# Performance work log

Measured on AMD Instinct MI355X. Metric: run time of the kernel, lower is better.

## Reference

```python
import jax, jax.numpy as jnp
import numpy as np

H = 8          # attention heads
EPS = 1e-5     # LayerNorm eps (torch default)
B, T, E = 8, 1024, 128
D, DI, N, DC, R = 512, 1024, 16, 4, 32   # d_model, d_inner, d_state, d_conv, dt_rank
NT, NM = 6, 8                            # transformer layers, mamba layers
FF = 2048                                # transformer dim_feedforward (torch default)


def setup_inputs():
    key = jax.random.key(0)
    ks = iter(jax.random.split(key, 48))
    def rn(shape, scale=0.05):
        return jax.random.normal(next(ks), shape, jnp.float32) * scale
    return {
        "emb":      jax.random.normal(next(ks), (B, T, E), jnp.float32),
        # TransformerEncoder (6 post-norm layers), params stacked on leading layer dim
        "t_wqkv":   rn((NT, 3 * E, E)), "t_bqkv": jnp.zeros((NT, 3 * E), jnp.float32),
        "t_wo":     rn((NT, E, E)),     "t_bo":   jnp.zeros((NT, E), jnp.float32),
        "t_ln1w":   jnp.ones((NT, E), jnp.float32),  "t_ln1b": jnp.zeros((NT, E), jnp.float32),
        "t_w1":     rn((NT, FF, E)),    "t_b1":   jnp.zeros((NT, FF), jnp.float32),
        "t_w2":     rn((NT, E, FF)),    "t_b2":   jnp.zeros((NT, E), jnp.float32),
        "t_ln2w":   jnp.ones((NT, E), jnp.float32),  "t_ln2b": jnp.zeros((NT, E), jnp.float32),
        # Linear(emb_dim -> d_model)
        "w_in":     rn((D, E)), "b_in": jnp.zeros((D,), jnp.float32),
        # MambaBlocks (8 raw Mamba layers, no residual/norm), stacked
        "m_inproj": rn((NM, 2 * DI, D)),
        "m_convw":  rn((NM, DI, DC), 0.2), "m_convb": jnp.zeros((NM, DI), jnp.float32),
        "m_xproj":  rn((NM, R + 2 * N, DI)),
        "m_dtw":    rn((NM, DI, R), 0.1),
        "m_dtb":    jax.random.uniform(next(ks), (NM, DI), jnp.float32, -6.0, -3.0),
        "m_Alog":   jnp.log(jnp.tile(jnp.arange(1, N + 1, dtype=jnp.float32), (NM, DI, 1))),
        "m_D":      jnp.ones((NM, DI), jnp.float32),
        "m_outproj": rn((NM, D, DI)),
        # Linear(d_model -> emb_dim)
        "w_out":    rn((E, D)), "b_out": jnp.zeros((E,), jnp.float32),
    }


def _ln(x, w, b):
    mu = jnp.mean(x, -1, keepdims=True)
    var = jnp.var(x, -1, keepdims=True)
    return (x - mu) * jax.lax.rsqrt(var + EPS) * w + b


def _tlayer(x, p):
    wqkv, bqkv, wo, bo, ln1w, ln1b, w1, b1, w2, b2, ln2w, ln2b = p
    qkv = x @ wqkv.T + bqkv                        # (B,T,3E)
    q, k, v = jnp.split(qkv, 3, axis=-1)
    def heads(t):                                  # (B,T,E) -> (B,H,T,E//H)
        return t.reshape(B, T, H, E // H).transpose(0, 2, 1, 3)
    q, k, v = heads(q), heads(k), heads(v)
    scores = jnp.einsum("bhqd,bhkd->bhqk", q, k) / jnp.sqrt(jnp.float32(E // H))
    attn = jax.nn.softmax(scores, axis=-1)
    o = jnp.einsum("bhqk,bhkd->bhqd", attn, v).transpose(0, 2, 1, 3).reshape(B, T, E)
    x = _ln(x + o @ wo.T + bo, ln1w, ln1b)         # post-norm (torch default)
    ff = jax.nn.relu(x @ w1.T + b1) @ w2.T + b2
    return _ln(x + ff, ln2w, ln2b)


def _mamba_layer(x, p):
    inproj, convw, convb, xproj, dtw, dtb, Alog, Dp, outproj = p
    xz = x @ inproj.T                              # (B,T,2*DI)
    xi, z = jnp.split(xz, 2, axis=-1)
    # causal depthwise conv1d, kernel DC, left-padded
    xp = jnp.pad(xi, ((0, 0), (DC - 1, 0), (0, 0)))
    conv = sum(xp[:, k:k + T, :] * convw[:, k] for k in range(DC)) + convb
    xi = jax.nn.silu(conv)
    dbc = xi @ xproj.T                             # (B,T,R+2N)
    dt_r, Bt, Ct = dbc[..., :R], dbc[..., R:R + N], dbc[..., R + N:]
    dt = jax.nn.softplus(dt_r @ dtw.T + dtb)       # (B,T,DI)
    A = -jnp.exp(Alog)                             # (DI,N)
    def step(h, inputs):
        dt_t, B_t, C_t, x_t = inputs               # (B,DI),(B,N),(B,N),(B,DI)
        dA = jnp.exp(dt_t[:, :, None] * A)         # (B,DI,N)
        h = h * dA + (dt_t * x_t)[:, :, None] * B_t[:, None, :]
        y = jnp.einsum("bdn,bn->bd", h, C_t)
        return h, y
    h0 = jnp.zeros((B, DI, N), x.dtype)
    seq = (dt.transpose(1, 0, 2), Bt.transpose(1, 0, 2),
           Ct.transpose(1, 0, 2), xi.transpose(1, 0, 2))
    _, ys = jax.lax.scan(step, h0, seq)            # ys: (T,B,DI)
    y = ys.transpose(1, 0, 2) + Dp * xi
    y = y * jax.nn.silu(z)
    return y @ outproj.T                           # (B,T,D)


def reference(emb, t_wqkv, t_bqkv, t_wo, t_bo, t_ln1w, t_ln1b, t_w1, t_b1, t_w2, t_b2,
              t_ln2w, t_ln2b, w_in, b_in, m_inproj, m_convw, m_convb, m_xproj, m_dtw,
              m_dtb, m_Alog, m_D, m_outproj, w_out, b_out):
    x = emb
    tparams = (t_wqkv, t_bqkv, t_wo, t_bo, t_ln1w, t_ln1b, t_w1, t_b1, t_w2, t_b2, t_ln2w, t_ln2b)
    for i in range(NT):
        x = _tlayer(x, tuple(p[i] for p in tparams))
    x = x @ w_in.T + b_in                          # (B,T,D)
    mparams = (m_inproj, m_convw, m_convb, m_xproj, m_dtw, m_dtb, m_Alog, m_D, m_outproj)
    for i in range(NM):
        x = _mamba_layer(x, tuple(p[i] for p in mparams))
    return x @ w_out.T + b_out                     # (B,T,E)
```

## Files before the change

kernel.cpp:

```cpp
#include <hip/hip_runtime.h>
#include <math.h>

#define HB 8
#define TT 1024
#define NSTATE 16
#define NTT 6
#define NMM 8
#define MM (HB*TT)
#define EPSV 1e-5f
#define CHUNK 64
#define NCH (TT/CHUNK)
#define AKS 128
#define VSTR 132

typedef _Float16 f16x8 __attribute__((ext_vector_type(8)));
typedef _Float16 f16x4 __attribute__((ext_vector_type(4)));
typedef float f32x4_t __attribute__((ext_vector_type(4)));

static __device__ __forceinline__ void split8(const float4 a, const float4 b,
                                              f16x8& h, f16x8& l)
{
  float x[8] = {a.x, a.y, a.z, a.w, b.x, b.y, b.z, b.w};
#pragma unroll
  for (int i = 0; i < 8; i++) {
    _Float16 hi = (_Float16)x[i];
    h[i] = hi;
    l[i] = (_Float16)(x[i] - (float)hi);
  }
}

static __device__ __forceinline__ void gload16(const _Float16* g, _Float16* l)
{
  __builtin_amdgcn_global_load_lds(
      (const __attribute__((address_space(1))) unsigned int*)g,
      (__attribute__((address_space(3))) unsigned int*)l, 16, 0, 0);
}

static __device__ __forceinline__ void store_split(_Float16* __restrict__ dst,
                                                   size_t row, int col, float v)
{
  const int cc = col & 31;
  const size_t o = ((size_t)(col >> 5) * MM + row) * 64
                 + (size_t)(((((cc >> 3) ^ ((int)row & 7)) * 8)) + (cc & 7));
  _Float16 hi = (_Float16)v;
  dst[o] = hi;
  dst[o ^ (size_t)32] = (_Float16)(v - (float)hi);
}

static __device__ __forceinline__ void split_item(
    const float* __restrict__ src, int lda, int rows,
    _Float16* __restrict__ dst, int item)
{
  const int m = item % rows;
  const int seg = item / rows;
  const float* s = src + (size_t)m * lda + seg * 32;
  _Float16* d = dst + (size_t)item * 64;
  const int swz = m & 7;
#pragma unroll
  for (int g = 0; g < 4; g++) {
    float4 x0 = *(const float4*)&s[g * 8];
    float4 x1 = *(const float4*)&s[g * 8 + 4];
    f16x8 h, l;
    split8(x0, x1, h, l);
    const int u = (g ^ swz) * 8;
    *(f16x8*)&d[u] = h;
    *(f16x8*)&d[u ^ 32] = l;
  }
}

__global__ __launch_bounds__(256) void split_k(
    const float* __restrict__ src, int lda, int rows,
    _Float16* __restrict__ dst)
{
  split_item(src, lda, rows, dst, blockIdx.x * 256 + threadIdx.x);
}

__global__ __launch_bounds__(256) void split3_k(
    const float* __restrict__ s0, int lda0, int rows0, _Float16* __restrict__ d0, int nb0,
    const float* __restrict__ s1, int lda1, int rows1, _Float16* __restrict__ d1, int nb1,
    const float* __restrict__ s2, int lda2, int rows2, _Float16* __restrict__ d2)
{
  const int bid = blockIdx.x;
  if (bid < nb0) {
    split_item(s0, lda0, rows0, d0, bid * 256 + threadIdx.x);
  } else if (bid < nb0 + nb1) {
    split_item(s1, lda1, rows1, d1, (bid - nb0) * 256 + threadIdx.x);
  } else {
    split_item(s2, lda2, rows2, d2, (bid - nb0 - nb1) * 256 + threadIdx.x);
  }
}

template<int TN>
__global__ __launch_bounds__(256, 4) void gemm_ps_t(
    const _Float16* __restrict__ Ap, int astr,
    const _Float16* __restrict__ Wp, int wstr,
    const float* __restrict__ bias,
    float* __restrict__ C,
    float* __restrict__ P,
    _Float16* __restrict__ Cs,
    int N, int K, int S, int act)
{
  __shared__ __align__(16) _Float16 As[128 * 64];
  __shared__ __align__(16) _Float16 Bs[TN * 64];
  const int tid = threadIdx.x;
  const int lane = tid & 63;
  const int w = tid >> 6;
  const int quad = lane >> 4;
  const int l16 = lane & 15;
  const int m0 = blockIdx.y * 128;
  const int n0 = blockIdx.x * TN;
  const int z = blockIdx.z;
  const int nseg = K / 32;
  const int segb = z * (nseg / S);
  const int sege = segb + nseg / S;

  constexpr int MI = (TN == 128) ? 4 : 2;
  const int w0 = (TN == 128) ? (w & 1) : w;
  const int w1 = (TN == 128) ? (w >> 1) : 0;
  const int rowbase = (TN == 128) ? w0 * 64 : w0 * 32;

  f32x4_t acc[MI][4];
#pragma unroll
  for (int i = 0; i < MI; i++)
#pragma unroll
    for (int j = 0; j < 4; j++)
#pragma unroll
      for (int r = 0; r < 4; r++) acc[i][j][r] = 0.f;

  const int sw8 = (quad ^ (l16 & 7)) * 8;
  const int abase = (rowbase + l16) * 64 + sw8;
  const int bbase = (w1 * 64 + l16) * 64 + sw8;
  const int wave64 = tid & 192;

  for (int seg = segb; seg < sege; seg++) {
    const _Float16* At = Ap + ((size_t)seg * astr + m0) * 64;
    const _Float16* Bt = Wp + ((size_t)seg * wstr + n0) * 64;
    __syncthreads();
#pragma unroll
    for (int j = 0; j < 4; j++)
      gload16(At + (size_t)(j * 256 + tid) * 8, &As[(j * 256 + wave64) * 8]);
#pragma unroll
    for (int j = 0; j < TN / 32; j++)
      gload16(Bt + (size_t)(j * 256 + tid) * 8, &Bs[(j * 256 + wave64) * 8]);
    __syncthreads();

    f16x8 bh[4], bl[4];
#pragma unroll
    for (int ni = 0; ni < 4; ni++) {
      bh[ni] = *(const f16x8*)&Bs[bbase + ni * 1024];
      bl[ni] = *(const f16x8*)&Bs[(bbase ^ 32) + ni * 1024];
    }
#pragma unroll
    for (int mi = 0; mi < MI; mi++) {
      f16x8 ah = *(const f16x8*)&As[abase + mi * 1024];
      f16x8 al = *(const f16x8*)&As[(abase ^ 32) + mi * 1024];
#pragma unroll
      for (int ni = 0; ni < 4; ni++) {
        acc[mi][ni] = __builtin_amdgcn_mfma_f32_16x16x32_f16(ah, bh[ni], acc[mi][ni], 0, 0, 0);
        acc[mi][ni] = __builtin_amdgcn_mfma_f32_16x16x32_f16(ah, bl[ni], acc[mi][ni], 0, 0, 0);
        acc[mi][ni] = __builtin_amdgcn_mfma_f32_16x16x32_f16(al, bh[ni], acc[mi][ni], 0, 0, 0);
      }
    }
  }

  float* dst = (S == 1) ? C : (P + (size_t)z * MM * N);
#pragma unroll
  for (int ni = 0; ni < 4; ni++) {
    const int n = n0 + w1 * 64 + ni * 16 + l16;
    const float bv = (S == 1 && bias) ? bias[n] : 0.f;
#pragma unroll
    for (int mi = 0; mi < MI; mi++) {
      const int mbase = m0 + rowbase + mi * 16 + quad * 4;
#pragma unroll
      for (int r = 0; r < 4; r++) {
        float v = acc[mi][ni][r] + bv;
        if (S == 1) {
          if (act == 1) v = fmaxf(v, 0.f);
          else if (act == 2) v = fmaxf(v, 0.f) + log1pf(__expf(-fabsf(v)));
        }
        const int row = mbase + r;
        if (S == 1 && Cs) {
          store_split(Cs, (size_t)row, n, v);
        } else {
          dst[(size_t)row * N + n] = v;
        }
      }
    }
  }
}

__global__ __launch_bounds__(256) void reduce_k(
    const float* __restrict__ P, const float* __restrict__ bias,
    float* __restrict__ C, _Float16* __restrict__ Cs,
    _Float16* __restrict__ dta,
    int nmask, int nshift, int S, int act, int stride4)
{
  const int idx = blockIdx.x * 256 + threadIdx.x;
  float4 a = *(const float4*)&P[(size_t)idx * 4];
  for (int z = 1; z < S; z++) {
    float4 p = *(const float4*)&P[(size_t)(idx + (size_t)z * stride4) * 4];
    a.x += p.x; a.y += p.y; a.z += p.z; a.w += p.w;
  }
  if (bias) {
    float4 bv = *(const float4*)&bias[(idx * 4) & nmask];
    a.x += bv.x; a.y += bv.y; a.z += bv.z; a.w += bv.w;
  }
  if (act == 1) {
    a.x = fmaxf(a.x, 0.f); a.y = fmaxf(a.y, 0.f);
    a.z = fmaxf(a.z, 0.f); a.w = fmaxf(a.w, 0.f);
  } else if (act == 2) {
    a.x = fmaxf(a.x, 0.f) + log1pf(__expf(-fabsf(a.x)));
    a.y = fmaxf(a.y, 0.f) + log1pf(__expf(-fabsf(a.y)));
    a.z = fmaxf(a.z, 0.f) + log1pf(__expf(-fabsf(a.z)));
    a.w = fmaxf(a.w, 0.f) + log1pf(__expf(-fabsf(a.w)));
  }
  const int c0 = (idx * 4) & nmask;
  const size_t row = (size_t)(idx * 4) >> nshift;
  if (Cs) {
    store_split(Cs, row, c0,     a.x);
    store_split(Cs, row, c0 + 1, a.y);
    store_split(Cs, row, c0 + 2, a.z);
    store_split(Cs, row, c0 + 3, a.w);
  } else {
    *(float4*)&C[(size_t)idx * 4] = a;
  }
  if (dta && c0 < 32) {
    store_split(dta, row, c0,     a.x);
    store_split(dta, row, c0 + 1, a.y);
    store_split(dta, row, c0 + 2, a.z);
    store_split(dta, row, c0 + 3, a.w);
  }
}

__global__ __launch_bounds__(256) void attn_mfma_k(
    const float* __restrict__ qkv, _Float16* __restrict__ os)
{
  __shared__ _Float16 Khi[AKS * 16], Klo[AKS * 16];
  __shared__ _Float16 Vthi[16 * VSTR], Vtlo[16 * VSTR];
  __shared__ float Pscr[4][16 * 18];

  const int tid = threadIdx.x;
  const int lane = tid & 63;
  const int wv = tid >> 6;
  const int quad = lane >> 4;
  const int l16 = lane & 15;
  const int qh = quad & 1;
  const int bh = blockIdx.y;
  const int b = bh >> 3;
  const int h = bh & 7;
  const int qb0 = blockIdx.x * 128;

  f16x8 qa[2];
#pragma unroll
  for (int u = 0; u < 2; u++) {
    const int qrow = qb0 + wv * 32 + u * 16 + l16;
    const float* qp = qkv + (size_t)(b * TT + qrow) * 384 + h * 16 + qh * 8;
    float4 x0 = *(const float4*)&qp[0];
    float4 x1 = *(const float4*)&qp[4];
    float xv[8] = {x0.x, x0.y, x0.z, x0.w, x1.x, x1.y, x1.z, x1.w};
#pragma unroll
    for (int j = 0; j < 8; j++) {
      float q = xv[j] * 0.25f;
      _Float16 hi = (_Float16)q;
      _Float16 lo = (_Float16)(q - (float)hi);
      qa[u][j] = (quad < 2) ? hi : lo;
    }
  }

  f32x4_t oacc[2];
  float lacc[2][4];
#pragma unroll
  for (int u = 0; u < 2; u++)
#pragma unroll
    for (int r = 0; r < 4; r++) { oacc[u][r] = 0.f; lacc[u][r] = 0.f; }

  float* Pw = &Pscr[wv][0];

  for (int ks = 0; ks < TT; ks += AKS) {
    __syncthreads();
    {
      const int key = tid >> 1, hf = tid & 1;
      const float* kp = qkv + (size_t)(b * TT + ks + key) * 384 + 128 + h * 16 + hf * 8;
      float4 k0 = *(const float4*)&kp[0];
      float4 k1 = *(const float4*)&kp[4];
      f16x8 vh, vl;
      split8(k0, k1, vh, vl);
      *(f16x8*)&Khi[key * 16 + hf * 8] = vh;
      *(f16x8*)&Klo[key * 16 + hf * 8] = vl;
      const float* vp = kp + 128;
      float4 v0 = *(const float4*)&vp[0];
      float4 v1 = *(const float4*)&vp[4];
      float vvv[8] = {v0.x, v0.y, v0.z, v0.w, v1.x, v1.y, v1.z, v1.w};
#pragma unroll
      for (int j = 0; j < 8; j++) {
        const int d = hf * 8 + j;
        _Float16 hi = (_Float16)vvv[j];
        Vthi[d * VSTR + key] = hi;
        Vtlo[d * VSTR + key] = (_Float16)(vvv[j] - (float)hi);
      }
    }
    __syncthreads();

    for (int kt = 0; kt < AKS; kt += 16) {
      f16x8 kfh = *(const f16x8*)&Khi[(kt + l16) * 16 + qh * 8];
      f16x8 kfl = *(const f16x8*)&Klo[(kt + l16) * 16 + qh * 8];
      const int vo = l16 * VSTR + kt + qh * 8;
      f16x4 va0 = *(const f16x4*)&Vthi[vo];
      f16x4 va1 = *(const f16x4*)&Vthi[vo + 4];
      f16x4 vb0 = *(const f16x4*)&Vtlo[vo];
      f16x4 vb1 = *(const f16x4*)&Vtlo[vo + 4];
      f16x8 vfh, vfl;
#pragma unroll
      for (int i = 0; i < 4; i++) {
        vfh[i] = va0[i]; vfh[4 + i] = va1[i];
        vfl[i] = vb0[i]; vfl[4 + i] = vb1[i];
      }

#pragma unroll
      for (int u = 0; u < 2; u++) {
        f32x4_t s;
#pragma unroll
        for (int r = 0; r < 4; r++) s[r] = 0.f;
        s = __builtin_amdgcn_mfma_f32_16x16x32_f16(qa[u], kfh, s, 0, 0, 0);
        s = __builtin_amdgcn_mfma_f32_16x16x32_f16(qa[u], kfl, s, 0, 0, 0);
        float p[4];
#pragma unroll
        for (int r = 0; r < 4; r++) {
          p[r] = __expf(s[r]);
          lacc[u][r] += p[r];
        }
        float* ps = Pw + (quad * 4) * 18 + l16;
        ps[0] = p[0]; ps[18] = p[1]; ps[36] = p[2]; ps[54] = p[3];
        __asm__ volatile("s_waitcnt lgkmcnt(0)" ::: "memory");
        const float* pr = Pw + l16 * 18 + qh * 8;
        f16x8 pa;
#pragma unroll
        for (int j = 0; j < 8; j++) {
          float pv = pr[j];
          _Float16 hi = (_Float16)pv;
          _Float16 lo = (_Float16)(pv - (float)hi);
          pa[j] = (quad < 2) ? hi : lo;
        }
        oacc[u] = __builtin_amdgcn_mfma_f32_16x16x32_f16(pa, vfh, oacc[u], 0, 0, 0);
        oacc[u] = __builtin_amdgcn_mfma_f32_16x16x32_f16(pa, vfl, oacc[u], 0, 0, 0);
        __asm__ volatile("s_waitcnt lgkmcnt(0)" ::: "memory");
      }
    }
  }

#pragma unroll
  for (int u = 0; u < 2; u++) {
#pragma unroll
    for (int r = 0; r < 4; r++) {
      float lv = lacc[u][r];
      lv += __shfl_xor(lv, 1);
      lv += __shfl_xor(lv, 2);
      lv += __shfl_xor(lv, 4);
      lv += __shfl_xor(lv, 8);
      const float inv = 1.f / lv;
      const int qrow = qb0 + wv * 32 + u * 16 + quad * 4 + r;
      const size_t m = (size_t)(b * TT + qrow);
      store_split(os, m, h * 16 + l16, oacc[u][r] * inv);
    }
  }
}

__global__ __launch_bounds__(256) void add_ln_k(
    const float* __restrict__ a, const float* __restrict__ bvec,
    const float* __restrict__ w, const float* __restrict__ bb,
    float* __restrict__ out, _Float16* __restrict__ outs)
{
  const int tid = threadIdx.x;
  const int wave = tid >> 6, lane = tid & 63;
  const size_t row = (size_t)blockIdx.x * 4 + wave;
  const float* pa = a + row * 128;
  const float* pb = bvec + row * 128;
  float v0 = pa[lane] + pb[lane];
  float v1 = pa[lane + 64] + pb[lane + 64];
  float s1 = v0 + v1, s2 = v0 * v0 + v1 * v1;
#pragma unroll
  for (int off = 32; off; off >>= 1) {
    s1 += __shfl_down(s1, off);
    s2 += __shfl_down(s2, off);
  }
  s1 = __shfl(s1, 0); s2 = __shfl(s2, 0);
  const float mean = s1 * (1.f / 128.f);
  const float var = s2 * (1.f / 128.f) - mean * mean;
  const float rs = rsqrtf(var + EPSV);
  const float o0 = (v0 - mean) * rs * w[lane] + bb[lane];
  const float o1 = (v1 - mean) * rs * w[lane + 64] + bb[lane + 64];
  out[row * 128 + lane] = o0;
  out[row * 128 + lane + 64] = o1;
  store_split(outs, row, lane, o0);
  store_split(outs, row, lane + 64, o1);
}

__global__ __launch_bounds__(256) void conv_silu_k(
    const float* __restrict__ xz, const float* __restrict__ cw,
    const float* __restrict__ cb, float* __restrict__ out,
    _Float16* __restrict__ outs)
{
  const int idx = blockIdx.x * 256 + threadIdx.x;
  const int di = idx & 1023;
  const int m = idx >> 10;
  const int t = m & (TT - 1);
  float acc = cb[di];
#pragma unroll
  for (int k = 0; k < 4; k++) {
    int tt = t + k - 3;
    if (tt >= 0) acc += xz[(size_t)(m + k - 3) * 2048 + di] * cw[di * 4 + k];
  }
  const float y = acc / (1.f + __expf(-acc));
  out[(size_t)m * 1024 + di] = y;
  store_split(outs, (size_t)m, di, y);
}

__global__ __launch_bounds__(64) void scan_partial_k(
    const float* __restrict__ dt,
    const float* __restrict__ dbc,
    const float* __restrict__ xi,
    const float* __restrict__ Alog,
    float* __restrict__ Pb, float* __restrict__ Sb)
{
  const int slice = blockIdx.x & 15;
  const int c = blockIdx.x >> 4;
  const int b = blockIdx.y;
  const int di = slice * 64 + threadIdx.x;

  float A[NSTATE];
#pragma unroll
  for (int n = 0; n < NSTATE; n++) A[n] = -__expf(Alog[di * NSTATE + n]);
  float h[NSTATE], P[NSTATE];
#pragma unroll
  for (int n = 0; n < NSTATE; n++) { h[n] = 0.f; P[n] = 1.f; }

  const size_t m0 = (size_t)b * TT + (size_t)c * CHUNK;
  for (int t = 0; t < CHUNK; t++) {
    const size_t m = m0 + t;
    const float dtv = dt[m * 1024 + di];
    const float xv  = xi[m * 1024 + di];
    const float dtx = dtv * xv;
#pragma unroll
    for (int n = 0; n < NSTATE; n++) {
      const float Bv = dbc[m * 64 + 32 + n];
      const float dA = __expf(dtv * A[n]);
      h[n] = h[n] * dA + dtx * Bv;
      P[n] *= dA;
    }
  }
  const size_t base = (((size_t)b * NCH + c) * NSTATE) * 1024 + di;
#pragma unroll
  for (int n = 0; n < NSTATE; n++) {
    Pb[base + (size_t)n * 1024] = P[n];
    Sb[base + (size_t)n * 1024] = h[n];
  }
}

__global__ __launch_bounds__(256) void scan_fix_k(
    float* __restrict__ Pb, const float* __restrict__ Sb)
{
  const int idx = blockIdx.x * 256 + threadIdx.x;
  const int b = idx >> 10;
  const int di = idx & 1023;
  float h[NSTATE];
#pragma unroll
  for (int n = 0; n < NSTATE; n++) h[n] = 0.f;
  for (int c = 0; c < NCH; c++) {
    const size_t base = (((size_t)b * NCH + c) * NSTATE) * 1024 + di;
    float P[NSTATE], S[NSTATE];
#pragma unroll
    for (int n = 0; n < NSTATE; n++) {
      P[n] = Pb[base + (size_t)n * 1024];
      S[n] = Sb[base + (size_t)n * 1024];
    }
#pragma unroll
    for (int n = 0; n < NSTATE; n++) {
      Pb[base + (size_t)n * 1024] = h[n];
      h[n] = P[n] * h[n] + S[n];
    }
  }
}

__global__ __launch_bounds__(64) void scan_final_k(
    const float* __restrict__ dt,
    const float* __restrict__ dbc,
    const float* __restrict__ xi,
    const float* __restrict__ xz,
    const float* __restrict__ Alog,
    const float* __restrict__ Dp,
    const float* __restrict__ Hin,
    _Float16* __restrict__ Y)
{
  const int slice = blockIdx.x & 15;
  const int c = blockIdx.x >> 4;
  const int b = blockIdx.y;
  const int di = slice * 64 + threadIdx.x;

  float A[NSTATE];
#pragma unroll
  for (int n = 0; n < NSTATE; n++) A[n] = -__expf(Alog[di * NSTATE + n]);
  const float Dv = Dp[di];
  float h[NSTATE];
  const size_t hbase = (((size_t)b * NCH + c) * NSTATE) * 1024 + di;
#pragma unroll
  for (int n = 0; n < NSTATE; n++) h[n] = Hin[hbase + (size_t)n * 1024];

  const size_t m0 = (size_t)b * TT + (size_t)c * CHUNK;
  for (int t = 0; t < CHUNK; t++) {
    const size_t m = m0 + t;
    const float dtv = dt[m * 1024 + di];
    const float xv  = xi[m * 1024 + di];
    const float zv  = xz[m * 2048 + 1024 + di];
    const float dtx = dtv * xv;
    float y = 0.f;
#pragma unroll
    for (int n = 0; n < NSTATE; n++) {
      const float Bv = dbc[m * 64 + 32 + n];
      const float Cv = dbc[m * 64 + 48 + n];
      const float dA = __expf(dtv * A[n]);
      h[n] = h[n] * dA + dtx * Bv;
      y += h[n] * Cv;
    }
    y += Dv * xv;
    y *= zv / (1.f + __expf(-zv));
    store_split(Y, m, di, y);
  }
}

extern "C" void kernel_launch(void* const* d_in, const int* in_sizes, int n_in,
                              void* d_out, int out_size, void* d_ws, size_t ws_size,
                              hipStream_t stream)
{
  (void)in_sizes; (void)n_in; (void)out_size; (void)ws_size;
  const float* emb      = (const float*)d_in[0];
  const float* t_wqkv   = (const float*)d_in[1];
  const float* t_bqkv   = (const float*)d_in[2];
  const float* t_wo     = (const float*)d_in[3];
  const float* t_bo     = (const float*)d_in[4];
  const float* t_ln1w   = (const float*)d_in[5];
  const float* t_ln1b   = (const float*)d_in[6];
  const float* t_w1     = (const float*)d_in[7];
  const float* t_b1     = (const float*)d_in[8];
  const float* t_w2     = (const float*)d_in[9];
  const float* t_b2     = (const float*)d_in[10];
  const float* t_ln2w   = (const float*)d_in[11];
  const float* t_ln2b   = (const float*)d_in[12];
  const float* w_in     = (const float*)d_in[13];
  const float* b_in     = (const float*)d_in[14];
  const float* m_inproj = (const float*)d_in[15];
  const float* m_convw  = (const float*)d_in[16];
  const float* m_convb  = (const float*)d_in[17];
  const float* m_xproj  = (const float*)d_in[18];
  const float* m_dtw    = (const float*)d_in[19];
  const float* m_dtb    = (const float*)d_in[20];
  const float* m_Alog   = (const float*)d_in[21];
  const float* m_D      = (const float*)d_in[22];
  const float* m_outproj= (const float*)d_in[23];
  const float* w_out    = (const float*)d_in[24];
  const float* b_out    = (const float*)d_in[25];

  float* ws = (float*)d_ws;
  float* R1 = ws;
  float* R2 = ws + (size_t)MM * 512;
  float* R3 = ws + (size_t)MM * 1024;
  float* R4 = ws + (size_t)MM * 3072;
  float* R5 = ws + (size_t)MM * 4096;
  float* R6 = ws + (size_t)MM * 5120;
  float* R7 = ws + (size_t)MM * 6144;

  _Float16* TWQKV = (_Float16*)R4;
  _Float16* TWO   = TWQKV + (size_t)294912 * 2;
  _Float16* TW1   = TWO   + (size_t)98304 * 2;
  _Float16* TW2   = TW1   + (size_t)1572864 * 2;
  _Float16* TWIN  = TW2   + (size_t)1572864 * 2;

  _Float16* ASP1 = (_Float16*)R6;
  _Float16* XIS  = (_Float16*)R6;
  _Float16* DTA  = (_Float16*)R6;
  _Float16* YSP  = (_Float16*)R6;

  dim3 blk(256);
  auto split = [&](const float* src, int lda, int rows, int K, _Float16* dst) {
    hipLaunchKernelGGL(split_k, dim3(rows * (K / 32) / 256), blk, 0, stream,
                       src, lda, rows, dst);
  };
  auto gemm = [&](const _Float16* Ap, const _Float16* Wp, int wstr,
                  const float* bias, float* C, int N, int K, int act,
                  int S, float* P, _Float16* Cs, _Float16* dta, bool tn64) {
    dim3 g(N / (tn64 ? 64 : 128), MM / 128, S);
    if (tn64)
      hipLaunchKernelGGL(gemm_ps_t<64>, g, blk, 0, stream,
                         Ap, MM, Wp, wstr, bias, C, P, Cs, N, K, S, act);
    else
      hipLaunchKernelGGL(gemm_ps_t<128>, g, blk, 0, stream,
                         Ap, MM, Wp, wstr, bias, C, P, Cs, N, K, S, act);
    if (S > 1) {
      int stride4 = (int)((size_t)MM * N / 4);
      hipLaunchKernelGGL(reduce_k, dim3(stride4 / 256), blk, 0, stream,
                         P, bias, C, Cs, dta, N - 1, __builtin_ctz(N), S, act,
                         stride4);
    }
  };

  split(t_wqkv, 128,  2304,  128, TWQKV);
  split(t_wo,   128,   768,  128, TWO);
  split(t_w1,   128, 12288,  128, TW1);
  split(t_w2,  2048,   768, 2048, TW2);
  split(w_in,   128,   512,  128, TWIN);
  split(emb,    128,    MM,  128, ASP1);

  const float* x = emb;
  for (int l = 0; l < NTT; l++) {
    gemm(ASP1, TWQKV + (size_t)l * 384 * 64, 2304, t_bqkv + l * 384,
         R3, 384, 128, 0, 1, nullptr, nullptr, nullptr, false);
    hipLaunchKernelGGL(attn_mfma_k, dim3(TT / 128, HB * 8), blk, 0, stream,
                       R3, ASP1);
    gemm(ASP1, TWO + (size_t)l * 128 * 64, 768, t_bo + l * 128,
         R5, 128, 128, 0, 2, R2, nullptr, nullptr, true);
    hipLaunchKernelGGL(add_ln_k, dim3(MM / 4), blk, 0, stream,
                       x, R5, t_ln1w + l * 128, t_ln1b + l * 128, R1, ASP1);
    gemm(ASP1, TW1 + (size_t)l * 2048 * 64, 12288, t_b1 + l * 2048,
         R3, 2048, 128, 1, 1, nullptr, (_Float16*)R3, nullptr, false);
    gemm((_Float16*)R3, TW2 + (size_t)l * 128 * 64, 768, t_b2 + l * 128,
         R5, 128, 2048, 0, 8, R6, nullptr, nullptr, false);
    hipLaunchKernelGGL(add_ln_k, dim3(MM / 4), blk, 0, stream,
                       R1, R5, t_ln2w + l * 128, t_ln2b + l * 128, R1, ASP1);
    x = R1;
  }

  gemm(ASP1, TWIN, 512, b_in, R2, 512, 128, 0, 1, nullptr, (_Float16*)R2,
       nullptr, false);

  float* xcs = R2;
  float* xos = R1;
  for (int l = 0; l < NMM; l++) {
    _Float16* WIs = (_Float16*)(xos + (size_t)MM * 256);
    _Float16* WXs = (_Float16*)(xos + (size_t)MM * 384);
    _Float16* WDs = (_Float16*)(xos + (size_t)MM * 392);
    _Float16* WOs = (_Float16*)(xos + (size_t)MM * 256);
    hipLaunchKernelGGL(split3_k, dim3(140), blk, 0, stream,
        m_inproj + (size_t)l * 2048 * 512, 512, 2048, WIs, 128,
        m_xproj  + (size_t)l * 64 * 1024, 1024,   64, WXs,   8,
        m_dtw    + (size_t)l * 1024 * 32,   32, 1024, WDs);

    gemm((_Float16*)xcs, WIs, 2048, nullptr,
         R3, 2048, 512, 0, 1, nullptr, nullptr, nullptr, false);
    hipLaunchKernelGGL(conv_silu_k, dim3(MM * 1024 / 256), blk, 0, stream,
                       R3, m_convw + (size_t)l * 1024 * 4, m_convb + l * 1024,
                       R4, XIS);
    gemm(XIS, WXs, 64, nullptr,
         R7, 64, 1024, 0, 4, xos, nullptr, DTA, true);
    gemm(DTA, WDs, 1024, m_dtb + l * 1024,
         R5, 1024, 32, 2, 1, nullptr, nullptr, nullptr, false);

    float* Pb = xos;
    float* Sb = xos + (size_t)MM * 256;
    hipLaunchKernelGGL(scan_partial_k, dim3(16 * NCH, HB), dim3(64), 0, stream,
                       R5, R7, R4, m_Alog + (size_t)l * 1024 * 16, Pb, Sb);
    hipLaunchKernelGGL(scan_fix_k, dim3(MM / 1024 * 4), blk, 0, stream, Pb, Sb);
    split(m_outproj + (size_t)l * 512 * 1024, 1024, 512, 1024, WOs);
    hipLaunchKernelGGL(scan_final_k, dim3(16 * NCH, HB), dim3(64), 0, stream,
                       R5, R7, R4, R3,
                       m_Alog + (size_t)l * 1024 * 16, m_D + l * 1024, Pb, YSP);

    gemm(YSP, WOs, 512, nullptr,
         R5, 512, 1024, 0, 2, R3, (_Float16*)xos, nullptr, false);
    float* ts = xcs; xcs = xos; xos = ts;
  }

  _Float16* WOUTs = (_Float16*)xos;
  split(w_out, 512, 128, 512, WOUTs);
  gemm((_Float16*)xcs, WOUTs, 128, b_out,
       (float*)d_out, 128, 512, 0, 4, R6, nullptr, nullptr, false);
}
```

Before: 3.779 ms.

## Pre-split K/V once per layer, async-load into attention, vectorize split stores

Adds a kv_split_k kernel that converts K and V to swizzled hi/lo fp16 layouts in global memory once per layer. The attention kernel then streams these tiles into LDS with global_load_lds instead of having every query block re-split K/V from fp32. It also merges the six initial weight and input split launches into one kernel, writes split pairs as f16x2 stores, and makes conv_silu handle two channels per thread. The cost is one extra kernel launch per transformer layer plus scratch buffers in R2.

After: 3.965 ms. 1.05x slower.

```diff
diff --git a/kernel.cpp b/kernel.cpp
--- a/kernel.cpp
+++ b/kernel.cpp
@@ -11,10 +11,11 @@
 #define CHUNK 64
 #define NCH (TT/CHUNK)
 #define AKS 128
-#define VSTR 132
+#define VST 136
 
 typedef _Float16 f16x8 __attribute__((ext_vector_type(8)));
 typedef _Float16 f16x4 __attribute__((ext_vector_type(4)));
+typedef _Float16 f16x2 __attribute__((ext_vector_type(2)));
 typedef float f32x4_t __attribute__((ext_vector_type(4)));
 
 static __device__ __forceinline__ void split8(const float4 a, const float4 b,
@@ -45,6 +46,20 @@
   _Float16 hi = (_Float16)v;
   dst[o] = hi;
   dst[o ^ (size_t)32] = (_Float16)(v - (float)hi);
+}
+
+static __device__ __forceinline__ void store_split2(_Float16* __restrict__ dst,
+                                                    size_t row, int col0,
+                                                    float v0, float v1)
+{
+  const int cc = col0 & 31;
+  const size_t o = ((size_t)(col0 >> 5) * MM + row) * 64
+                 + (size_t)(((((cc >> 3) ^ ((int)row & 7)) * 8)) + (cc & 7));
+  _Float16 h0 = (_Float16)v0, h1 = (_Float16)v1;
+  f16x2 hp = {h0, h1};
+  f16x2 lp = {(_Float16)(v0 - (float)h0), (_Float16)(v1 - (float)h1)};
+  *(f16x2*)&dst[o] = hp;
+  *(f16x2*)&dst[o ^ (size_t)32] = lp;
 }
 
 static __device__ __forceinline__ void split_item(
@@ -87,6 +102,73 @@
     split_item(s1, lda1, rows1, d1, (bid - nb0) * 256 + threadIdx.x);
   } else {
     split_item(s2, lda2, rows2, d2, (bid - nb0 - nb1) * 256 + threadIdx.x);
+  }
+}
+
+__global__ __launch_bounds__(256) void split6_k(
+    const float* __restrict__ s0, int lda0, int rows0, _Float16* __restrict__ d0, int c0,
+    const float* __restrict__ s1, int lda1, int rows1, _Float16* __restrict__ d1, int c1,
+    const float* __restrict__ s2, int lda2, int rows2, _Float16* __restrict__ d2, int c2,
+    const float* __restrict__ s3, int lda3, int rows3, _Float16* __restrict__ d3, int c3,
+    const float* __restrict__ s4, int lda4, int rows4, _Float16* __restrict__ d4, int c4,
+    const float* __restrict__ s5, int lda5, int rows5, _Float16* __restrict__ d5)
+{
+  const int bid = blockIdx.x;
+  if (bid < c0)      split_item(s0, lda0, rows0, d0, bid * 256 + threadIdx.x);
+  else if (bid < c1) split_item(s1, lda1, rows1, d1, (bid - c0) * 256 + threadIdx.x);
+  else if (bid < c2) split_item(s2, lda2, rows2, d2, (bid - c1) * 256 + threadIdx.x);
+  else if (bid < c3) split_item(s3, lda3, rows3, d3, (bid - c2) * 256 + threadIdx.x);
+  else if (bid < c4) split_item(s4, lda4, rows4, d4, (bid - c3) * 256 + threadIdx.x);
+  else               split_item(s5, lda5, rows5, d5, (bid - c4) * 256 + threadIdx.x);
+}
+
+__global__ __launch_bounds__(256) void kv_split_k(
+    const float* __restrict__ qkv,
+    _Float16* __restrict__ Ks, _Float16* __restrict__ Vs)
+{
+  __shared__ _Float16 Vthi[16 * VST], Vtlo[16 * VST];
+  const int tid = threadIdx.x;
+  const int bh = blockIdx.y;
+  const int b = bh >> 3;
+  const int h = bh & 7;
+  const int kb0 = blockIdx.x * 128;
+
+  const int kl = tid >> 1;
+  const int half = tid & 1;
+  const int key = kb0 + kl;
+  const float* kp = qkv + (size_t)(b * TT + key) * 384 + 128 + h * 16 + half * 8;
+
+  {
+    float4 k0 = *(const float4*)&kp[0];
+    float4 k1 = *(const float4*)&kp[4];
+    f16x8 hh, ll;
+    split8(k0, k1, hh, ll);
+    const int p = (half + (key >> 1)) & 3;
+    _Float16* kb = Ks + (((size_t)bh << 10) + key) * 32;
+    *(f16x8*)&kb[p * 8] = hh;
+    *(f16x8*)&kb[(p ^ 2) * 8] = ll;
+  }
+  {
+    float4 v0 = *(const float4*)&kp[128];
+    float4 v1 = *(const float4*)&kp[132];
+    float xv[8] = {v0.x, v0.y, v0.z, v0.w, v1.x, v1.y, v1.z, v1.w};
+#pragma unroll
+    for (int j = 0; j < 8; j++) {
+      const int d = half * 8 + j;
+      _Float16 hi = (_Float16)xv[j];
+      Vthi[d * VST + kl] = hi;
+      Vtlo[d * VST + kl] = (_Float16)(xv[j] - (float)hi);
+    }
+  }
+  __syncthreads();
+  {
+    const int d = tid >> 4;
+    const int kg = tid & 15;
+    f16x8 hh = *(const f16x8*)&Vthi[d * VST + kg * 8];
+    f16x8 ll = *(const f16x8*)&Vtlo[d * VST + kg * 8];
+    _Float16* vb = Vs + ((size_t)bh * 32 + d) * 1024 + kb0 + ((kg ^ d) * 8);
+    *(f16x8*)&vb[0] = hh;
+    *(f16x8*)&vb[16 * 1024] = ll;
   }
 }
 
@@ -217,26 +299,25 @@
   const int c0 = (idx * 4) & nmask;
   const size_t row = (size_t)(idx * 4) >> nshift;
   if (Cs) {
-    store_split(Cs, row, c0,     a.x);
-    store_split(Cs, row, c0 + 1, a.y);
-    store_split(Cs, row, c0 + 2, a.z);
-    store_split(Cs, row, c0 + 3, a.w);
+    store_split2(Cs, row, c0,     a.x, a.y);
+    store_split2(Cs, row, c0 + 2, a.z, a.w);
   } else {
     *(float4*)&C[(size_t)idx * 4] = a;
   }
   if (dta && c0 < 32) {
-    store_split(dta, row, c0,     a.x);
-    store_split(dta, row, c0 + 1, a.y);
-    store_split(dta, row, c0 + 2, a.z);
-    store_split(dta, row, c0 + 3, a.w);
+    store_split2(dta, row, c0,     a.x, a.y);
+    store_split2(dta, row, c0 + 2, a.z, a.w);
   }
 }
 
 __global__ __launch_bounds__(256) void attn_mfma_k(
-    const float* __restrict__ qkv, _Float16* __restrict__ os)
-{
-  __shared__ _Float16 Khi[AKS * 16], Klo[AKS * 16];
-  __shared__ _Float16 Vthi[16 * VSTR], Vtlo[16 * VSTR];
+    const float* __restrict__ qkv,
+    const _Float16* __restrict__ Kg,
+    const _Float16* __restrict__ Vg,
+    _Float16* __restrict__ os)
+{
+  __shared__ __align__(16) _Float16 Klds[AKS * 32];
+  __shared__ __align__(16) _Float16 Vlds[32 * AKS];
   __shared__ float Pscr[4][16 * 18];
 
   const int tid = threadIdx.x;
@@ -249,6 +330,7 @@
   const int b = bh >> 3;
   const int h = bh & 7;
   const int qb0 = blockIdx.x * 128;
+  const int wave64 = tid & 192;
 
   f16x8 qa[2];
 #pragma unroll
@@ -275,46 +357,36 @@
     for (int r = 0; r < 4; r++) { oacc[u][r] = 0.f; lacc[u][r] = 0.f; }
 
   float* Pw = &Pscr[wv][0];
+  const _Float16* Kb = Kg + (((size_t)bh) << 10) * 32;
+  const _Float16* Vb = Vg + ((size_t)bh * 32) * 1024;
 
   for (int ks = 0; ks < TT; ks += AKS) {
     __syncthreads();
     {
-      const int key = tid >> 1, hf = tid & 1;
-      const float* kp = qkv + (size_t)(b * TT + ks + key) * 384 + 128 + h * 16 + hf * 8;
-      float4 k0 = *(const float4*)&kp[0];
-      float4 k1 = *(const float4*)&kp[4];
-      f16x8 vh, vl;
-      split8(k0, k1, vh, vl);
-      *(f16x8*)&Khi[key * 16 + hf * 8] = vh;
-      *(f16x8*)&Klo[key * 16 + hf * 8] = vl;
-      const float* vp = kp + 128;
-      float4 v0 = *(const float4*)&vp[0];
-      float4 v1 = *(const float4*)&vp[4];
-      float vvv[8] = {v0.x, v0.y, v0.z, v0.w, v1.x, v1.y, v1.z, v1.w};
-#pragma unroll
-      for (int j = 0; j < 8; j++) {
-        const int d = hf * 8 + j;
-        _Float16 hi = (_Float16)vvv[j];
-        Vthi[d * VSTR + key] = hi;
-        Vtlo[d * VSTR + key] = (_Float16)(vvv[j] - (float)hi);
+      const _Float16* Kt = Kb + (size_t)ks * 32;
+#pragma unroll
+      for (int it = 0; it < 2; it++) {
+        const int cb = it * 256 + tid;
+        gload16(Kt + (size_t)cb * 8, &Klds[(it * 256 + wave64) * 8]);
       }
+#pragma unroll
+      for (int it = 0; it < 2; it++) {
+        const int cb = it * 256 + tid;
+        const int rowv = cb >> 4, co = cb & 15;
+        gload16(Vb + (size_t)rowv * 1024 + ks + co * 8,
+                &Vlds[(it * 256 + wave64) * 8]);
+      }
     }
     __syncthreads();
 
     for (int kt = 0; kt < AKS; kt += 16) {
-      f16x8 kfh = *(const f16x8*)&Khi[(kt + l16) * 16 + qh * 8];
-      f16x8 kfl = *(const f16x8*)&Klo[(kt + l16) * 16 + qh * 8];
-      const int vo = l16 * VSTR + kt + qh * 8;
-      f16x4 va0 = *(const f16x4*)&Vthi[vo];
-      f16x4 va1 = *(const f16x4*)&Vthi[vo + 4];
-      f16x4 vb0 = *(const f16x4*)&Vtlo[vo];
-      f16x4 vb1 = *(const f16x4*)&Vtlo[vo + 4];
-      f16x8 vfh, vfl;
-#pragma unroll
-      for (int i = 0; i < 4; i++) {
-        vfh[i] = va0[i]; vfh[4 + i] = va1[i];
-        vfl[i] = vb0[i]; vfl[4 + i] = vb1[i];
-      }
+      const int key = kt + l16;
+      const int ph = (qh + (key >> 1)) & 3;
+      f16x8 kfh = *(const f16x8*)&Klds[key * 32 + ph * 8];
+      f16x8 kfl = *(const f16x8*)&Klds[key * 32 + (ph ^ 2) * 8];
+      const int vko = (kt + qh * 8) ^ (l16 * 8);
+      f16x8 vfh = *(const f16x8*)&Vlds[l16 * 128 + vko];
+      f16x8 vfl = *(const f16x8*)&Vlds[(16 + l16) * 128 + vko];
 
 #pragma unroll
       for (int u = 0; u < 2; u++) {
@@ -401,18 +473,24 @@
     _Float16* __restrict__ outs)
 {
   const int idx = blockIdx.x * 256 + threadIdx.x;
-  const int di = idx & 1023;
-  const int m = idx >> 10;
+  const int di = (idx & 511) * 2;
+  const int m = idx >> 9;
   const int t = m & (TT - 1);
-  float acc = cb[di];
+  float a0 = cb[di], a1 = cb[di + 1];
 #pragma unroll
   for (int k = 0; k < 4; k++) {
     int tt = t + k - 3;
-    if (tt >= 0) acc += xz[(size_t)(m + k - 3) * 2048 + di] * cw[di * 4 + k];
-  }
-  const float y = acc / (1.f + __expf(-acc));
-  out[(size_t)m * 1024 + di] = y;
-  store_split(outs, (size_t)m, di, y);
+    if (tt >= 0) {
+      float2 xv = *(const float2*)&xz[(size_t)(m + k - 3) * 2048 + di];
+      a0 += xv.x * cw[di * 4 + k];
+      a1 += xv.y * cw[(di + 1) * 4 + k];
+    }
+  }
+  const float y0 = a0 / (1.f + __expf(-a0));
+  const float y1 = a1 / (1.f + __expf(-a1));
+  float2 yo = {y0, y1};
+  *(float2*)&out[(size_t)m * 1024 + di] = yo;
+  store_split2(outs, (size_t)m, di, y0, y1);
 }
 
 __global__ __launch_bounds__(64) void scan_partial_k(
@@ -579,6 +657,9 @@
   _Float16* DTA  = (_Float16*)R6;
   _Float16* YSP  = (_Float16*)R6;
 
+  _Float16* KG = (_Float16*)(R2 + (size_t)MM * 256);
+  _Float16* VG = (_Float16*)(R2 + (size_t)MM * 320);
+
   dim3 blk(256);
   auto split = [&](const float* src, int lda, int rows, int K, _Float16* dst) {
     hipLaunchKernelGGL(split_k, dim3(rows * (K / 32) / 256), blk, 0, stream,
@@ -602,19 +683,22 @@
     }
   };
 
-  split(t_wqkv, 128,  2304,  128, TWQKV);
-  split(t_wo,   128,   768,  128, TWO);
-  split(t_w1,   128, 12288,  128, TW1);
-  split(t_w2,  2048,   768, 2048, TW2);
-  split(w_in,   128,   512,  128, TWIN);
-  split(emb,    128,    MM,  128, ASP1);
+  hipLaunchKernelGGL(split6_k, dim3(568), blk, 0, stream,
+      t_wqkv, 128,  2304, TWQKV,  36,
+      t_wo,   128,   768, TWO,    48,
+      t_w1,   128, 12288, TW1,   240,
+      t_w2,  2048,   768, TW2,   432,
+      w_in,   128,   512, TWIN,  440,
+      emb,    128,    MM, ASP1);
 
   const float* x = emb;
   for (int l = 0; l < NTT; l++) {
     gemm(ASP1, TWQKV + (size_t)l * 384 * 64, 2304, t_bqkv + l * 384,
          R3, 384, 128, 0, 1, nullptr, nullptr, nullptr, false);
+    hipLaunchKernelGGL(kv_split_k, dim3(8, HB * 8), blk, 0, stream,
+                       R3, KG, VG);
     hipLaunchKernelGGL(attn_mfma_k, dim3(TT / 128, HB * 8), blk, 0, stream,
-                       R3, ASP1);
+                       R3, KG, VG, ASP1);
     gemm(ASP1, TWO + (size_t)l * 128 * 64, 768, t_bo + l * 128,
          R5, 128, 128, 0, 2, R2, nullptr, nullptr, true);
     hipLaunchKernelGGL(add_ln_k, dim3(MM / 4), blk, 0, stream,
@@ -645,7 +729,7 @@
 
     gemm((_Float16*)xcs, WIs, 2048, nullptr,
          R3, 2048, 512, 0, 1, nullptr, nullptr, nullptr, false);
-    hipLaunchKernelGGL(conv_silu_k, dim3(MM * 1024 / 256), blk, 0, stream,
+    hipLaunchKernelGGL(conv_silu_k, dim3(MM * 512 / 256), blk, 0, stream,
                        R3, m_convw + (size_t)l * 1024 * 4, m_convb + l * 1024,
                        R4, XIS);
     gemm(XIS, WXs, 64, nullptr,
```
